# Kernel optimization log

Hardware: AMD Instinct MI355X
Metric: run time of the kernel (lower is better)

## Reference

```python
import jax, jax.numpy as jnp
import numpy as np

D, H, COND, MLP_RATIO = 1024, 16, 1024, 4
HD = D // H
DFF = MLP_RATIO * D


def layer_norm(x, w, eps=1e-5):
    xf = x.astype(jnp.float32)
    mu = jnp.mean(xf, axis=-1, keepdims=True)
    var = jnp.mean((xf - mu) ** 2, axis=-1, keepdims=True)
    return (xf - mu) * jax.lax.rsqrt(var + eps) * w


def rms_norm(x, w, eps=1e-6):
    xf = x.astype(jnp.float32)
    rms = jnp.sqrt(jnp.mean(xf * xf, axis=-1, keepdims=True) + eps)
    return (xf / rms * w).astype(x.dtype)


def rotate_half(x):
    x1, x2 = x[..., : x.shape[-1] // 2], x[..., x.shape[-1] // 2:]
    return jnp.concatenate([-x2, x1], axis=-1)


def apply_rope(x, cos, sin):
    return x * cos + rotate_half(x) * sin


def setup_inputs() -> dict:
    key = jax.random.key(0)
    ks = jax.random.split(key, 16)
    B, S = 4, 2048
    pos = jnp.arange(S, dtype=jnp.float32)
    inv = 1.0 / (10000.0 ** (jnp.arange(0, HD, 2, dtype=jnp.float32) / HD))
    freqs = pos[:, None] * inv[None, :]              # (S, HD/2)
    emb = jnp.concatenate([freqs, freqs], axis=-1)   # (S, HD)
    return {
        "x": jax.random.normal(ks[0], (B, S, D), jnp.float32),
        "cos": jnp.cos(emb)[None, :, None, :],        # (1,S,1,HD)
        "sin": jnp.sin(emb)[None, :, None, :],
        "c": jax.random.normal(ks[1], (B, COND), jnp.float32),
        "norm1_w": jnp.ones((D,), jnp.float32),
        "Wqkv": jax.random.normal(ks[2], (D, 3 * D), jnp.float32) * 0.02,
        "Wout": jax.random.normal(ks[3], (D, D), jnp.float32) * 0.02,
        "q_norm_w": jnp.ones((HD,), jnp.float32),
        "k_norm_w": jnp.ones((HD,), jnp.float32),
        "norm2_w": jnp.ones((D,), jnp.float32),
        "W1": jax.random.normal(ks[4], (D, DFF), jnp.float32) * 0.02,
        "b1": jnp.zeros((DFF,), jnp.float32),
        "W2": jax.random.normal(ks[5], (DFF, D), jnp.float32) * 0.02,
        "b2": jnp.zeros((D,), jnp.float32),
        "ada_W": jax.random.normal(ks[6], (COND, 6 * D), jnp.float32) * 0.02,
        "ada_b": jnp.zeros((6 * D,), jnp.float32),
    }


def reference(x, cos, sin, c, norm1_w, Wqkv, Wout, q_norm_w, k_norm_w,
              norm2_w, W1, b1, W2, b2, ada_W, ada_b):
    B, S, _ = x.shape
    mod = (c @ ada_W + ada_b)[:, None, :]            # (B,1,6D)
    sh_msa, sc_msa, g_msa, sh_mlp, sc_mlp, g_mlp = jnp.split(mod, 6, axis=-1)

    x_norm = layer_norm(x, norm1_w) * (1 + sc_msa) + sh_msa
    qkv = (x_norm @ Wqkv).reshape(B, S, 3, H, HD)
    q, k, v = qkv[:, :, 0], qkv[:, :, 1], qkv[:, :, 2]  # (B,S,H,HD)
    q = apply_rope(rms_norm(q, q_norm_w), cos, sin)
    k = apply_rope(rms_norm(k, k_norm_w), cos, sin)

    scale = 1.0 / jnp.sqrt(jnp.float32(HD))
    logits = jnp.einsum('bqhd,bkhd->bhqk', q, k) * scale
    probs = jax.nn.softmax(logits, axis=-1)
    attn = jnp.einsum('bhqk,bkhd->bqhd', probs, v).reshape(B, S, D)

    x = x + g_msa * (attn @ Wout)

    x_norm = layer_norm(x, norm2_w) * (1 + sc_mlp) + sh_mlp
    h = jax.nn.gelu(x_norm @ W1 + b1, approximate=True)
    x = x + g_mlp * (h @ W2 + b2)
    return x
```

## Files before the change

kernel.cpp:

```cpp
#include <hip/hip_runtime.h>
#include <hip/hip_bf16.h>
#include <math.h>

typedef __bf16 bf16;
typedef __bf16 bf16x8 __attribute__((ext_vector_type(8)));
typedef __bf16 bf16x4 __attribute__((ext_vector_type(4)));
typedef float f32x4 __attribute__((ext_vector_type(4)));

#define S_LEN 2048
#define NTOK 8192
#define DIM 1024
#define NH 16
#define HEADD 64
#define DFF 4096
#define MODD 6144

__device__ __forceinline__ void gload_lds16(const bf16* g, bf16* l) {
  __builtin_amdgcn_global_load_lds(
      (const __attribute__((address_space(1))) void*)g,
      (__attribute__((address_space(3))) void*)l, 16, 0, 0);
}

__device__ __forceinline__ float gelu_tanh(float x) {
  float inner = 0.7978845608028654f * (x + 0.044715f * x * x * x);
  return 0.5f * x * (1.0f + tanhf(inner));
}

__global__ __launch_bounds__(256) void init_mod_kernel(
    const float* __restrict__ ada_b, float* __restrict__ mod) {
  int i = blockIdx.x * 256 + threadIdx.x;
  mod[i] = ada_b[i % MODD];
}

__global__ __launch_bounds__(256) void ada_gemm_kernel(
    const float* __restrict__ cnd, const float* __restrict__ W,
    float* __restrict__ mod) {
  int n = blockIdx.x * 256 + threadIdx.x;
  int k0 = blockIdx.y * 128;
  float a0 = 0.f, a1 = 0.f, a2 = 0.f, a3 = 0.f;
  for (int k = k0; k < k0 + 128; ++k) {
    float w = W[(size_t)k * MODD + n];
    a0 = fmaf(cnd[k], w, a0);
    a1 = fmaf(cnd[1024 + k], w, a1);
    a2 = fmaf(cnd[2048 + k], w, a2);
    a3 = fmaf(cnd[3072 + k], w, a3);
  }
  atomicAdd(&mod[n], a0);
  atomicAdd(&mod[MODD + n], a1);
  atomicAdd(&mod[2 * MODD + n], a2);
  atomicAdd(&mod[3 * MODD + n], a3);
}

__global__ __launch_bounds__(256) void transpose_cast_kernel(
    const float* __restrict__ W, bf16* __restrict__ Wt, int K, int N) {
  __shared__ float tile[32][33];
  int n0 = blockIdx.x * 32, k0 = blockIdx.y * 32;
  int r = threadIdx.x >> 3;
  int c4 = (threadIdx.x & 7) * 4;
  float4 v = *(const float4*)&W[(size_t)(k0 + r) * N + n0 + c4];
  tile[r][c4 + 0] = v.x; tile[r][c4 + 1] = v.y;
  tile[r][c4 + 2] = v.z; tile[r][c4 + 3] = v.w;
  __syncthreads();
  bf16x4 o;
  o[0] = (bf16)tile[c4 + 0][r];
  o[1] = (bf16)tile[c4 + 1][r];
  o[2] = (bf16)tile[c4 + 2][r];
  o[3] = (bf16)tile[c4 + 3][r];
  *(bf16x4*)&Wt[(size_t)(n0 + r) * K + k0 + c4] = o;
}

__global__ __launch_bounds__(256) void vtrans_kernel(
    const bf16* __restrict__ qkv, bf16* __restrict__ VT) {
  __shared__ __align__(16) bf16 t[64][72];
  const int bh = blockIdx.y;
  const int b = bh >> 4, h = bh & 15;
  const int s0 = blockIdx.x * 64;
  const int tid = threadIdx.x;
  {
    const int r = tid >> 2;
    const int c = (tid & 3) * 16;
    const bf16* src =
        qkv + (size_t)(b * S_LEN + s0 + r) * 3072 + 2048 + h * 64 + c;
    *(bf16x8*)&t[r][c] = *(const bf16x8*)src;
    *(bf16x8*)&t[r][c + 8] = *(const bf16x8*)(src + 8);
  }
  __syncthreads();
  {
    const int d = tid & 63;
    const int sc = (tid >> 6) * 16;
    bf16x8 o0, o1;
#pragma unroll
    for (int j = 0; j < 8; ++j) o0[j] = t[sc + j][d];
#pragma unroll
    for (int j = 0; j < 8; ++j) o1[j] = t[sc + 8 + j][d];
    bf16* dst = VT + (size_t)(bh * 64 + d) * S_LEN + s0 + sc;
    *(bf16x8*)dst = o0;
    *(bf16x8*)(dst + 8) = o1;
  }
}

__global__ __launch_bounds__(256) void ln_mod_kernel(
    const float* __restrict__ x, const float* __restrict__ w,
    const float* __restrict__ mod, int sh_off, int sc_off,
    bf16* __restrict__ out) {
  __shared__ float red[8];
  const int row = blockIdx.x;
  const int b = row >> 11;
  const int tid = threadIdx.x;
  const float4 v = ((const float4*)(x + (size_t)row * DIM))[tid];
  float s1 = v.x + v.y + v.z + v.w;
  float s2 = v.x * v.x + v.y * v.y + v.z * v.z + v.w * v.w;
  for (int off = 32; off > 0; off >>= 1) {
    s1 += __shfl_down(s1, off, 64);
    s2 += __shfl_down(s2, off, 64);
  }
  const int wid = tid >> 6;
  if ((tid & 63) == 0) { red[wid] = s1; red[4 + wid] = s2; }
  __syncthreads();
  s1 = red[0] + red[1] + red[2] + red[3];
  s2 = red[4] + red[5] + red[6] + red[7];
  const float mu = s1 * (1.0f / DIM);
  const float inv = rsqrtf(s2 * (1.0f / DIM) - mu * mu + 1e-5f);
  const int c = tid * 4;
  const float* mb = mod + (size_t)b * MODD;
  float xs[4] = {v.x, v.y, v.z, v.w};
  bf16x4 o;
#pragma unroll
  for (int j = 0; j < 4; ++j)
    o[j] = (bf16)(((xs[j] - mu) * inv) * w[c + j] * (1.0f + mb[sc_off + c + j]) +
                  mb[sh_off + c + j]);
  *(bf16x4*)(out + (size_t)row * DIM + c) = o;
}

template <int EPI>
__global__ __launch_bounds__(256) void gemm_bt(
    const bf16* __restrict__ A, const bf16* __restrict__ Bt,
    bf16* __restrict__ Cb, float* __restrict__ Cf,
    const float* __restrict__ bias, const float* __restrict__ gmod,
    const float* __restrict__ resid, int M, int N, int K) {
  __shared__ __align__(16) bf16 As[128 * 32];
  __shared__ __align__(16) bf16 Bs[128 * 32];
  const int tid = threadIdx.x;
  const int wid = tid >> 6;
  const int lane = tid & 63;
  const int l15 = lane & 15;
  const int quad = lane >> 4;
  const int m0 = blockIdx.y * 128;
  const int n0 = blockIdx.x * 128;
  const int wm = (wid & 1) * 64;
  const int wn = (wid >> 1) * 64;

  const int r0 = tid >> 2;
  const int cc0 = (tid & 3) * 8;
  const size_t a_base = (size_t)(m0 + r0) * K + cc0;
  const size_t a_base2 = (size_t)(m0 + 64 + r0) * K + cc0;
  const size_t b_base = (size_t)(n0 + r0) * K + cc0;
  const size_t b_base2 = (size_t)(n0 + 64 + r0) * K + cc0;
  bf16* As_d = &As[tid * 8];
  bf16* As_d2 = &As[(256 + tid) * 8];
  bf16* Bs_d = &Bs[tid * 8];
  bf16* Bs_d2 = &Bs[(256 + tid) * 8];

  f32x4 acc[4][4] = {};

  for (int kt = 0; kt < K; kt += 32) {
    gload_lds16(A + a_base + kt, As_d);
    gload_lds16(A + a_base2 + kt, As_d2);
    gload_lds16(Bt + b_base + kt, Bs_d);
    gload_lds16(Bt + b_base2 + kt, Bs_d2);
    __syncthreads();
    bf16x8 af[4], bfr[4];
#pragma unroll
    for (int i = 0; i < 4; ++i) {
      af[i] = *(const bf16x8*)&As[(wm + i * 16 + l15) * 32 + quad * 8];
      bfr[i] = *(const bf16x8*)&Bs[(wn + i * 16 + l15) * 32 + quad * 8];
    }
#pragma unroll
    for (int i = 0; i < 4; ++i)
#pragma unroll
      for (int j = 0; j < 4; ++j)
        acc[i][j] = __builtin_amdgcn_mfma_f32_16x16x32_bf16(af[i], bfr[j],
                                                            acc[i][j], 0, 0, 0);
    __syncthreads();
  }

#pragma unroll
  for (int i = 0; i < 4; ++i) {
#pragma unroll
    for (int r = 0; r < 4; ++r) {
      const int m = m0 + wm + i * 16 + quad * 4 + r;
#pragma unroll
      for (int j = 0; j < 4; ++j) {
        const int n = n0 + wn + j * 16 + l15;
        float v = acc[i][j][r];
        if (EPI == 0) {
          Cb[(size_t)m * N + n] = (bf16)v;
        } else if (EPI == 1) {
          const int b = m >> 11;
          Cf[(size_t)m * N + n] =
              resid[(size_t)m * N + n] + gmod[(size_t)b * MODD + n] * v;
        } else if (EPI == 2) {
          v += bias[n];
          Cb[(size_t)m * N + n] = (bf16)gelu_tanh(v);
        } else {
          v += bias[n];
          const int b = m >> 11;
          Cf[(size_t)m * N + n] =
              resid[(size_t)m * N + n] + gmod[(size_t)b * MODD + n] * v;
        }
      }
    }
  }
}

__global__ __launch_bounds__(256) void rope_kernel(
    bf16* __restrict__ qkv, const float* __restrict__ cosb,
    const float* __restrict__ sinb, const float* __restrict__ qw,
    const float* __restrict__ kw) {
  const int wid = threadIdx.x >> 6;
  const int lane = threadIdx.x & 63;
  const int inst = blockIdx.x * 4 + wid;
  const int h = inst & (NH - 1);
  const int token = inst >> 4;
  const int s = token & (S_LEN - 1);
  const size_t base = (size_t)token * (3 * DIM) + h * HEADD + lane;
  const float cv = cosb[s * HEADD + lane];
  const float sv = sinb[s * HEADD + lane];
  const float sign = (lane < 32) ? -1.0f : 1.0f;
  {
    float xq = (float)qkv[base];
    float ss = xq * xq;
    for (int off = 1; off < 64; off <<= 1) ss += __shfl_xor(ss, off, 64);
    float rn = rsqrtf(ss * (1.0f / HEADD) + 1e-6f);
    float xn = xq * rn * qw[lane];
    float other = __shfl_xor(xn, 32, 64);
    qkv[base] = (bf16)(xn * cv + sign * other * sv);
  }
  {
    float xk = (float)qkv[base + DIM];
    float ss = xk * xk;
    for (int off = 1; off < 64; off <<= 1) ss += __shfl_xor(ss, off, 64);
    float rn = rsqrtf(ss * (1.0f / HEADD) + 1e-6f);
    float xn = xk * rn * kw[lane];
    float other = __shfl_xor(xn, 32, 64);
    qkv[base + DIM] = (bf16)(xn * cv + sign * other * sv);
  }
}

__global__ __launch_bounds__(256) void attn_kernel(
    const bf16* __restrict__ qkv, const bf16* __restrict__ VT,
    bf16* __restrict__ out) {
  __shared__ __align__(16) bf16 Ks[64][72];
  __shared__ __align__(16) bf16 Vs[64][72];
  __shared__ __align__(16) bf16 Ps[4][16][72];
  const int bh = blockIdx.y;
  const int b = bh >> 4;
  const int h = bh & 15;
  const int q0 = blockIdx.x * 64;
  const int tid = threadIdx.x;
  const int wid = tid >> 6;
  const int lane = tid & 63;
  const int l15 = lane & 15;
  const int quad = lane >> 4;

  const int qrow = q0 + wid * 16 + l15;
  const size_t qbase = (size_t)(b * S_LEN + qrow) * (3 * DIM) + h * HEADD;
  const bf16x8 aq0 = *(const bf16x8*)(qkv + qbase + quad * 8);
  const bf16x8 aq1 = *(const bf16x8*)(qkv + qbase + 32 + quad * 8);

  const int sr = tid >> 3;
  const int sc8 = (tid & 7) * 8;
  const float cexp = 0.125f * 1.44269504f;

  f32x4 oacc[4] = {};
  float psum[4] = {0.f, 0.f, 0.f, 0.f};

  for (int kt = 0; kt < S_LEN; kt += 64) {
    __syncthreads();
#pragma unroll
    for (int rep = 0; rep < 2; ++rep) {
      const int r = rep * 32 + sr;
      *(bf16x8*)&Ks[r][sc8] = *(const bf16x8*)(
          qkv + (size_t)(b * S_LEN + kt + r) * (3 * DIM) + DIM + h * HEADD + sc8);
      *(bf16x8*)&Vs[r][sc8] = *(const bf16x8*)(
          VT + (size_t)(bh * 64 + r) * S_LEN + kt + sc8);
    }
    __syncthreads();

    f32x4 sc[4] = {};
#pragma unroll
    for (int cc = 0; cc < 4; ++cc) {
      const bf16x8 b0 = *(const bf16x8*)&Ks[cc * 16 + l15][quad * 8];
      const bf16x8 b1 = *(const bf16x8*)&Ks[cc * 16 + l15][32 + quad * 8];
      sc[cc] = __builtin_amdgcn_mfma_f32_16x16x32_bf16(aq0, b0, sc[cc], 0, 0, 0);
      sc[cc] = __builtin_amdgcn_mfma_f32_16x16x32_bf16(aq1, b1, sc[cc], 0, 0, 0);
    }

#pragma unroll
    for (int cc = 0; cc < 4; ++cc) {
#pragma unroll
      for (int r = 0; r < 4; ++r) {
        const float p = __builtin_amdgcn_exp2f(fmaf(sc[cc][r], cexp, -8.0f));
        psum[r] += p;
        Ps[wid][quad * 4 + r][cc * 16 + l15] = (bf16)p;
      }
    }

    const bf16x8 pa0 = *(const bf16x8*)&Ps[wid][l15][quad * 8];
    const bf16x8 pa1 = *(const bf16x8*)&Ps[wid][l15][32 + quad * 8];
#pragma unroll
    for (int j = 0; j < 4; ++j) {
      const bf16x8 v0 = *(const bf16x8*)&Vs[j * 16 + l15][quad * 8];
      const bf16x8 v1 = *(const bf16x8*)&Vs[j * 16 + l15][32 + quad * 8];
      oacc[j] = __builtin_amdgcn_mfma_f32_16x16x32_bf16(pa0, v0, oacc[j], 0, 0, 0);
      oacc[j] = __builtin_amdgcn_mfma_f32_16x16x32_bf16(pa1, v1, oacc[j], 0, 0, 0);
    }
  }

#pragma unroll
  for (int r = 0; r < 4; ++r) {
    float ps = psum[r];
#pragma unroll
    for (int off = 1; off < 16; off <<= 1) ps += __shfl_xor(ps, off, 64);
    psum[r] = ps;
  }

#pragma unroll
  for (int r = 0; r < 4; ++r) {
    const int m = q0 + wid * 16 + quad * 4 + r;
    const float invl = 1.0f / psum[r];
#pragma unroll
    for (int j = 0; j < 4; ++j)
      out[((size_t)(b * S_LEN + m) * NH + h) * HEADD + j * 16 + l15] =
          (bf16)(oacc[j][r] * invl);
  }
}

extern "C" void kernel_launch(void* const* d_in, const int* in_sizes, int n_in,
                              void* d_out, int out_size, void* d_ws,
                              size_t ws_size, hipStream_t stream) {
  const float* x = (const float*)d_in[0];
  const float* cosb = (const float*)d_in[1];
  const float* sinb = (const float*)d_in[2];
  const float* cnd = (const float*)d_in[3];
  const float* norm1_w = (const float*)d_in[4];
  const float* Wqkv = (const float*)d_in[5];
  const float* Wout = (const float*)d_in[6];
  const float* q_norm_w = (const float*)d_in[7];
  const float* k_norm_w = (const float*)d_in[8];
  const float* norm2_w = (const float*)d_in[9];
  const float* W1 = (const float*)d_in[10];
  const float* b1 = (const float*)d_in[11];
  const float* W2 = (const float*)d_in[12];
  const float* b2 = (const float*)d_in[13];
  const float* ada_W = (const float*)d_in[14];
  const float* ada_b = (const float*)d_in[15];
  float* out = (float*)d_out;

  char* p = (char*)d_ws;
  float* mod = (float*)p;   p += (size_t)4 * MODD * 4;
  bf16* WqkvT = (bf16*)p;   p += (size_t)3072 * 1024 * 2;
  bf16* WoutT = (bf16*)p;   p += (size_t)1024 * 1024 * 2;
  bf16* W1T = (bf16*)p;     p += (size_t)4096 * 1024 * 2;
  bf16* W2T = (bf16*)p;     p += (size_t)1024 * 4096 * 2;
  bf16* XN = (bf16*)p;      p += (size_t)NTOK * DIM * 2;
  bf16* QKV = (bf16*)p;     p += (size_t)NTOK * 3 * DIM * 2;
  bf16* ATTN = (bf16*)p;    p += (size_t)NTOK * DIM * 2;
  bf16* Hbuf = (bf16*)p;    p += (size_t)NTOK * DFF * 2;
  bf16* VT = Hbuf;

  init_mod_kernel<<<96, 256, 0, stream>>>(ada_b, mod);
  ada_gemm_kernel<<<dim3(24, 8), 256, 0, stream>>>(cnd, ada_W, mod);
  transpose_cast_kernel<<<dim3(96, 32), 256, 0, stream>>>(Wqkv, WqkvT, 1024, 3072);
  transpose_cast_kernel<<<dim3(32, 32), 256, 0, stream>>>(Wout, WoutT, 1024, 1024);
  transpose_cast_kernel<<<dim3(128, 32), 256, 0, stream>>>(W1, W1T, 1024, 4096);
  transpose_cast_kernel<<<dim3(32, 128), 256, 0, stream>>>(W2, W2T, 4096, 1024);
  ln_mod_kernel<<<NTOK, 256, 0, stream>>>(x, norm1_w, mod, 0, 1024, XN);
  gemm_bt<0><<<dim3(24, 64), 256, 0, stream>>>(XN, WqkvT, QKV, nullptr, nullptr,
                                               nullptr, nullptr, NTOK, 3072, 1024);
  rope_kernel<<<NTOK * NH / 4, 256, 0, stream>>>(QKV, cosb, sinb, q_norm_w, k_norm_w);
  vtrans_kernel<<<dim3(32, 64), 256, 0, stream>>>(QKV, VT);
  attn_kernel<<<dim3(32, 64), 256, 0, stream>>>(QKV, VT, ATTN);
  gemm_bt<1><<<dim3(8, 64), 256, 0, stream>>>(ATTN, WoutT, nullptr, out, nullptr,
                                              mod + 2 * 1024, x, NTOK, 1024, 1024);
  ln_mod_kernel<<<NTOK, 256, 0, stream>>>(out, norm2_w, mod, 3 * 1024, 4 * 1024, XN);
  gemm_bt<2><<<dim3(32, 64), 256, 0, stream>>>(XN, W1T, Hbuf, nullptr, b1, nullptr,
                                               nullptr, NTOK, DFF, 1024);
  gemm_bt<3><<<dim3(8, 64), 256, 0, stream>>>(Hbuf, W2T, nullptr, out, b2,
                                              mod + 5 * 1024, out, NTOK, 1024, DFF);
  (void)in_sizes; (void)n_in; (void)out_size; (void)ws_size;
}
```

Before: 723.0 us.

## Deepen GEMM k-step to 64 and double attention query rows per block

The GEMM main loop now loads two 32-wide k-slices per iteration into two LDS buffers, which halves the number of barrier pairs per tile and keeps more loads in flight. The attention kernel now has each wave handle 32 query rows instead of 16, so every K/V tile staged in LDS serves twice as many queries and the grid is halved. The cost is more LDS and registers per block, which can lower occupancy, and the attention launch has fewer blocks.

```diff
diff --git a/kernel.cpp b/kernel.cpp
--- a/kernel.cpp
+++ b/kernel.cpp
@@ -138,8 +138,8 @@
     bf16* __restrict__ Cb, float* __restrict__ Cf,
     const float* __restrict__ bias, const float* __restrict__ gmod,
     const float* __restrict__ resid, int M, int N, int K) {
-  __shared__ __align__(16) bf16 As[128 * 32];
-  __shared__ __align__(16) bf16 Bs[128 * 32];
+  __shared__ __align__(16) bf16 As[2][128 * 32];
+  __shared__ __align__(16) bf16 Bs[2][128 * 32];
   const int tid = threadIdx.x;
   const int wid = tid >> 6;
   const int lane = tid & 63;
@@ -156,31 +156,34 @@
   const size_t a_base2 = (size_t)(m0 + 64 + r0) * K + cc0;
   const size_t b_base = (size_t)(n0 + r0) * K + cc0;
   const size_t b_base2 = (size_t)(n0 + 64 + r0) * K + cc0;
-  bf16* As_d = &As[tid * 8];
-  bf16* As_d2 = &As[(256 + tid) * 8];
-  bf16* Bs_d = &Bs[tid * 8];
-  bf16* Bs_d2 = &Bs[(256 + tid) * 8];
 
   f32x4 acc[4][4] = {};
 
-  for (int kt = 0; kt < K; kt += 32) {
-    gload_lds16(A + a_base + kt, As_d);
-    gload_lds16(A + a_base2 + kt, As_d2);
-    gload_lds16(Bt + b_base + kt, Bs_d);
-    gload_lds16(Bt + b_base2 + kt, Bs_d2);
+  for (int kt = 0; kt < K; kt += 64) {
+    gload_lds16(A + a_base + kt, &As[0][tid * 8]);
+    gload_lds16(A + a_base2 + kt, &As[0][(256 + tid) * 8]);
+    gload_lds16(Bt + b_base + kt, &Bs[0][tid * 8]);
+    gload_lds16(Bt + b_base2 + kt, &Bs[0][(256 + tid) * 8]);
+    gload_lds16(A + a_base + kt + 32, &As[1][tid * 8]);
+    gload_lds16(A + a_base2 + kt + 32, &As[1][(256 + tid) * 8]);
+    gload_lds16(Bt + b_base + kt + 32, &Bs[1][tid * 8]);
+    gload_lds16(Bt + b_base2 + kt + 32, &Bs[1][(256 + tid) * 8]);
     __syncthreads();
-    bf16x8 af[4], bfr[4];
-#pragma unroll
-    for (int i = 0; i < 4; ++i) {
-      af[i] = *(const bf16x8*)&As[(wm + i * 16 + l15) * 32 + quad * 8];
-      bfr[i] = *(const bf16x8*)&Bs[(wn + i * 16 + l15) * 32 + quad * 8];
-    }
-#pragma unroll
-    for (int i = 0; i < 4; ++i)
-#pragma unroll
-      for (int j = 0; j < 4; ++j)
-        acc[i][j] = __builtin_amdgcn_mfma_f32_16x16x32_bf16(af[i], bfr[j],
-                                                            acc[i][j], 0, 0, 0);
+#pragma unroll
+    for (int half = 0; half < 2; ++half) {
+      bf16x8 af[4], bfr[4];
+#pragma unroll
+      for (int i = 0; i < 4; ++i) {
+        af[i] = *(const bf16x8*)&As[half][(wm + i * 16 + l15) * 32 + quad * 8];
+        bfr[i] = *(const bf16x8*)&Bs[half][(wn + i * 16 + l15) * 32 + quad * 8];
+      }
+#pragma unroll
+      for (int i = 0; i < 4; ++i)
+#pragma unroll
+        for (int j = 0; j < 4; ++j)
+          acc[i][j] = __builtin_amdgcn_mfma_f32_16x16x32_bf16(af[i], bfr[j],
+                                                              acc[i][j], 0, 0, 0);
+    }
     __syncthreads();
   }
 
@@ -252,28 +255,32 @@
     bf16* __restrict__ out) {
   __shared__ __align__(16) bf16 Ks[64][72];
   __shared__ __align__(16) bf16 Vs[64][72];
-  __shared__ __align__(16) bf16 Ps[4][16][72];
+  __shared__ __align__(16) bf16 Ps[4][32][72];
   const int bh = blockIdx.y;
   const int b = bh >> 4;
   const int h = bh & 15;
-  const int q0 = blockIdx.x * 64;
+  const int q0 = blockIdx.x * 128;
   const int tid = threadIdx.x;
   const int wid = tid >> 6;
   const int lane = tid & 63;
   const int l15 = lane & 15;
   const int quad = lane >> 4;
 
-  const int qrow = q0 + wid * 16 + l15;
-  const size_t qbase = (size_t)(b * S_LEN + qrow) * (3 * DIM) + h * HEADD;
-  const bf16x8 aq0 = *(const bf16x8*)(qkv + qbase + quad * 8);
-  const bf16x8 aq1 = *(const bf16x8*)(qkv + qbase + 32 + quad * 8);
+  bf16x8 aq[2][2];
+#pragma unroll
+  for (int i = 0; i < 2; ++i) {
+    const int qrow = q0 + wid * 32 + i * 16 + l15;
+    const size_t qbase = (size_t)(b * S_LEN + qrow) * (3 * DIM) + h * HEADD;
+    aq[i][0] = *(const bf16x8*)(qkv + qbase + quad * 8);
+    aq[i][1] = *(const bf16x8*)(qkv + qbase + 32 + quad * 8);
+  }
 
   const int sr = tid >> 3;
   const int sc8 = (tid & 7) * 8;
   const float cexp = 0.125f * 1.44269504f;
 
-  f32x4 oacc[4] = {};
-  float psum[4] = {0.f, 0.f, 0.f, 0.f};
+  f32x4 oacc[2][4] = {};
+  float psum[2][4] = {{0.f, 0.f, 0.f, 0.f}, {0.f, 0.f, 0.f, 0.f}};
 
   for (int kt = 0; kt < S_LEN; kt += 64) {
     __syncthreads();
@@ -287,53 +294,61 @@
     }
     __syncthreads();
 
-    f32x4 sc[4] = {};
+    f32x4 sc[2][4] = {};
 #pragma unroll
     for (int cc = 0; cc < 4; ++cc) {
       const bf16x8 b0 = *(const bf16x8*)&Ks[cc * 16 + l15][quad * 8];
       const bf16x8 b1 = *(const bf16x8*)&Ks[cc * 16 + l15][32 + quad * 8];
-      sc[cc] = __builtin_amdgcn_mfma_f32_16x16x32_bf16(aq0, b0, sc[cc], 0, 0, 0);
-      sc[cc] = __builtin_amdgcn_mfma_f32_16x16x32_bf16(aq1, b1, sc[cc], 0, 0, 0);
-    }
-
-#pragma unroll
-    for (int cc = 0; cc < 4; ++cc) {
-#pragma unroll
-      for (int r = 0; r < 4; ++r) {
-        const float p = __builtin_amdgcn_exp2f(fmaf(sc[cc][r], cexp, -8.0f));
-        psum[r] += p;
-        Ps[wid][quad * 4 + r][cc * 16 + l15] = (bf16)p;
+#pragma unroll
+      for (int i = 0; i < 2; ++i) {
+        sc[i][cc] = __builtin_amdgcn_mfma_f32_16x16x32_bf16(aq[i][0], b0, sc[i][cc], 0, 0, 0);
+        sc[i][cc] = __builtin_amdgcn_mfma_f32_16x16x32_bf16(aq[i][1], b1, sc[i][cc], 0, 0, 0);
       }
     }
 
-    const bf16x8 pa0 = *(const bf16x8*)&Ps[wid][l15][quad * 8];
-    const bf16x8 pa1 = *(const bf16x8*)&Ps[wid][l15][32 + quad * 8];
+#pragma unroll
+    for (int i = 0; i < 2; ++i)
+#pragma unroll
+      for (int cc = 0; cc < 4; ++cc)
+#pragma unroll
+        for (int r = 0; r < 4; ++r) {
+          const float p = __builtin_amdgcn_exp2f(fmaf(sc[i][cc][r], cexp, -8.0f));
+          psum[i][r] += p;
+          Ps[wid][i * 16 + quad * 4 + r][cc * 16 + l15] = (bf16)p;
+        }
+
+    bf16x8 pa[2][2];
+#pragma unroll
+    for (int i = 0; i < 2; ++i) {
+      pa[i][0] = *(const bf16x8*)&Ps[wid][i * 16 + l15][quad * 8];
+      pa[i][1] = *(const bf16x8*)&Ps[wid][i * 16 + l15][32 + quad * 8];
+    }
 #pragma unroll
     for (int j = 0; j < 4; ++j) {
       const bf16x8 v0 = *(const bf16x8*)&Vs[j * 16 + l15][quad * 8];
       const bf16x8 v1 = *(const bf16x8*)&Vs[j * 16 + l15][32 + quad * 8];
-      oacc[j] = __builtin_amdgcn_mfma_f32_16x16x32_bf16(pa0, v0, oacc[j], 0, 0, 0);
-      oacc[j] = __builtin_amdgcn_mfma_f32_16x16x32_bf16(pa1, v1, oacc[j], 0, 0, 0);
-    }
-  }
-
-#pragma unroll
-  for (int r = 0; r < 4; ++r) {
-    float ps = psum[r];
-#pragma unroll
-    for (int off = 1; off < 16; off <<= 1) ps += __shfl_xor(ps, off, 64);
-    psum[r] = ps;
-  }
-
-#pragma unroll
-  for (int r = 0; r < 4; ++r) {
-    const int m = q0 + wid * 16 + quad * 4 + r;
-    const float invl = 1.0f / psum[r];
-#pragma unroll
-    for (int j = 0; j < 4; ++j)
-      out[((size_t)(b * S_LEN + m) * NH + h) * HEADD + j * 16 + l15] =
-          (bf16)(oacc[j][r] * invl);
-  }
+#pragma unroll
+      for (int i = 0; i < 2; ++i) {
+        oacc[i][j] = __builtin_amdgcn_mfma_f32_16x16x32_bf16(pa[i][0], v0, oacc[i][j], 0, 0, 0);
+        oacc[i][j] = __builtin_amdgcn_mfma_f32_16x16x32_bf16(pa[i][1], v1, oacc[i][j], 0, 0, 0);
+      }
+    }
+  }
+
+#pragma unroll
+  for (int i = 0; i < 2; ++i)
+#pragma unroll
+    for (int r = 0; r < 4; ++r) {
+      float ps = psum[i][r];
+#pragma unroll
+      for (int off = 1; off < 16; off <<= 1) ps += __shfl_xor(ps, off, 64);
+      const int m = q0 + wid * 32 + i * 16 + quad * 4 + r;
+      const float invl = 1.0f / ps;
+#pragma unroll
+      for (int j = 0; j < 4; ++j)
+        out[((size_t)(b * S_LEN + m) * NH + h) * HEADD + j * 16 + l15] =
+            (bf16)(oacc[i][j][r] * invl);
+    }
 }
 
 extern "C" void kernel_launch(void* const* d_in, const int* in_sizes, int n_in,
@@ -380,7 +395,7 @@
                                                nullptr, nullptr, NTOK, 3072, 1024);
   rope_kernel<<<NTOK * NH / 4, 256, 0, stream>>>(QKV, cosb, sinb, q_norm_w, k_norm_w);
   vtrans_kernel<<<dim3(32, 64), 256, 0, stream>>>(QKV, VT);
-  attn_kernel<<<dim3(32, 64), 256, 0, stream>>>(QKV, VT, ATTN);
+  attn_kernel<<<dim3(16, 64), 256, 0, stream>>>(QKV, VT, ATTN);
   gemm_bt<1><<<dim3(8, 64), 256, 0, stream>>>(ATTN, WoutT, nullptr, out, nullptr,
                                               mod + 2 * 1024, x, NTOK, 1024, 1024);
   ln_mod_kernel<<<NTOK, 256, 0, stream>>>(out, norm2_w, mod, 3 * 1024, 4 * 1024, XN);
```

Measured after the change: 684.2 us. 5.4% less time.
